# Optimization experiments

Hardware: AMD Instinct MI355X
Metric: run time of the kernel (lower is better)

## Reference

```python
import jax, jax.numpy as jnp
import numpy as np

B, T, C, H = 32, 512, 8, 256  # batch, seq_len, n_channels, HIDDEN_SIZE
G = 4 * H  # gate dim (i, f, g, o)


def setup_inputs() -> dict:
    key = jax.random.key(0)
    ks = jax.random.split(key, 12)
    k_scale = 1.0 / np.sqrt(H)  # PyTorch LSTM/Linear uniform init bound
    u = lambda k, shape: jax.random.uniform(k, shape, jnp.float32, -k_scale, k_scale)
    return {
        "x": jax.random.normal(ks[0], (B, T, C), jnp.float32),
        # per-channel LSTM layer 1 (input_size=1)
        "Wih1": u(ks[1], (C, G, 1)),
        "Whh1": u(ks[2], (C, G, H)),
        "bih1": u(ks[3], (C, G)),
        "bhh1": u(ks[4], (C, G)),
        # per-channel LSTM layer 2 (input_size=H)
        "Wih2": u(ks[5], (C, G, H)),
        "Whh2": u(ks[6], (C, G, H)),
        "bih2": u(ks[7], (C, G)),
        "bhh2": u(ks[8], (C, G)),
        # per-channel Linear(H, 1)
        "Wlin": u(ks[9], (C, H)),
        "blin": u(ks[10], (C,)),
    }


def _lstm_layer(x_proj, Whh):
    """x_proj: [T, C, B, 4H] precomputed input projection + biases.
    Whh: [C, 4H, H]. Returns hidden states [T, C, B, H]."""
    c_dim, b_dim = x_proj.shape[1], x_proj.shape[2]
    h0 = jnp.zeros((c_dim, b_dim, H), x_proj.dtype)
    c0 = jnp.zeros((c_dim, b_dim, H), x_proj.dtype)

    def step(carry, xp_t):
        h, c = carry
        gates = xp_t + jnp.einsum('cbh,cgh->cbg', h, Whh)
        i, f, g, o = jnp.split(gates, 4, axis=-1)  # PyTorch gate order i,f,g,o
        i = jax.nn.sigmoid(i)
        f = jax.nn.sigmoid(f)
        g = jnp.tanh(g)
        o = jax.nn.sigmoid(o)
        c_new = f * c + i * g
        h_new = o * jnp.tanh(c_new)
        return (h_new, c_new), h_new

    _, hs = jax.lax.scan(step, (h0, c0), x_proj)
    return hs  # [T, C, B, H]


def reference(x, Wih1, Whh1, bih1, bhh1, Wih2, Whh2, bih2, bhh2, Wlin, blin):
    # Dropout layers are identity in eval mode.
    # Layer 1: input_size=1 -> input projection is a per-channel scale of x.
    b1 = (bih1 + bhh1)[None, :, None, :]  # [1, C, 1, 4H]
    xp1 = jnp.einsum('btc,cg->tcbg', x, Wih1[:, :, 0]) + b1  # [T, C, B, 4H]
    h1 = _lstm_layer(xp1, Whh1)  # [T, C, B, H]

    # Layer 2
    b2 = (bih2 + bhh2)[None, :, None, :]
    xp2 = jnp.einsum('tcbh,cgh->tcbg', h1, Wih2) + b2
    h2 = _lstm_layer(xp2, Whh2)  # [T, C, B, H]

    # Per-channel Linear(H, 1), concatenated over channel dim.
    out = jnp.einsum('tcbh,ch->btc', h2, Wlin) + blin[None, None, :]
    return out  # [B, T, C]
```

## Files before the change

### kernel.cpp

```cpp
#include <hip/hip_runtime.h>

#define Bn 32
#define Tn 512
#define Cn 8
#define Hn 256
#define Gn 1024
#define NTHR 128
#define SLC  32
#define NBLK (Cn*2*SLC)
#define K2n  (Hn/2)
#define EXU3 (3*Cn*K2n*Bn)
#define GP2  18

typedef __attribute__((ext_vector_type(8))) __bf16 bf16x8;
typedef __attribute__((ext_vector_type(8))) short  short8;
typedef __attribute__((ext_vector_type(4))) float  f32x4;
typedef __attribute__((ext_vector_type(4))) unsigned uintx4;
typedef unsigned long long u64;

__device__ __forceinline__ unsigned bfr(float f) {
    unsigned u = __float_as_uint(f);
    return (u + 0x7fffu + ((u >> 16) & 1u)) >> 16;
}
__device__ __forceinline__ float sigmf(float v)  { return 1.0f / (1.0f + __expf(-v)); }
__device__ __forceinline__ float tanh_f(float v) { return 1.0f - 2.0f / (__expf(2.0f * v) + 1.0f); }

__device__ __forceinline__ f32x4 mf(short8 a, short8 b, f32x4 c) {
    return __builtin_amdgcn_mfma_f32_16x16x32_bf16(
        __builtin_bit_cast(bf16x8, a), __builtin_bit_cast(bf16x8, b), c, 0, 0, 0);
}

__device__ __forceinline__ void splitw(const float* __restrict__ p, short8& hi, short8& lo) {
    short8 h, l;
#pragma unroll
    for (int j = 0; j < 8; ++j) {
        const float v = p[j];
        const unsigned hb = bfr(v);
        h[j] = (short)hb;
        l[j] = (short)bfr(v - __uint_as_float(hb << 16));
    }
    hi = h; lo = l;
}

__device__ __forceinline__ void ast64(u64* p, u64 v) {
    __hip_atomic_store(p, v, __ATOMIC_RELAXED, __HIP_MEMORY_SCOPE_AGENT);
}
__device__ __forceinline__ u64 ald64(const u64* p) {
    return __hip_atomic_load(p, __ATOMIC_RELAXED, __HIP_MEMORY_SCOPE_AGENT);
}

__global__ void __launch_bounds__(NTHR, 1)
lstm_mfma(const float* __restrict__ x,
          const float* __restrict__ Wih1, const float* __restrict__ Whh1,
          const float* __restrict__ bih1, const float* __restrict__ bhh1,
          const float* __restrict__ Wih2, const float* __restrict__ Whh2,
          const float* __restrict__ bih2, const float* __restrict__ bhh2,
          const float* __restrict__ Wlin, const float* __restrict__ blin,
          float* __restrict__ out, void* __restrict__ wsv, int use_part) {
    __shared__ float g1buf[2 * 32 * GP2];
    __shared__ float g2buf[2 * 32 * GP2];

    u64* EX1 = (u64*)wsv;
    u64* EX2 = EX1 + EXU3;
    float* part = (float*)(EX2 + EXU3);

    const int tid  = threadIdx.x;
    const int wg   = blockIdx.x;
    const int c    = wg & 7;
    const int bh   = (wg >> 8) & 1;
    const int s    = (wg >> 3) & 31;
    const int lane = tid & 63;
    const int kg   = tid >> 6;
    const int n    = lane & 15;
    const int quad = lane >> 4;
    const int bn   = bh * 16 + n;

    short8 w1h[2][4], w1l[2][4], w2h[2][4], w2l[2][4], w3h[2][4], w3l[2][4];
#pragma unroll
    for (int mt = 0; mt < 2; ++mt) {
        const int r = mt * 16 + n;
        const size_t g = (size_t)((r >> 3) * Hn + s * 8 + (r & 7));
        const size_t base = (size_t)c * Gn * Hn + g * Hn + kg * 128 + quad * 8;
#pragma unroll
        for (int kk = 0; kk < 4; ++kk) {
            splitw(Whh1 + base + kk * 32, w1h[mt][kk], w1l[mt][kk]);
            splitw(Wih2 + base + kk * 32, w2h[mt][kk], w2l[mt][kk]);
            splitw(Whh2 + base + kk * 32, w3h[mt][kk], w3l[mt][kk]);
        }
    }

    float wi1_r[2][4], bs1_r[2][4], bs2_r[2][4];
#pragma unroll
    for (int mt = 0; mt < 2; ++mt)
#pragma unroll
        for (int reg = 0; reg < 4; ++reg) {
            const int r = mt * 16 + quad * 4 + reg;
            const int g = (r >> 3) * Hn + s * 8 + (r & 7);
            wi1_r[mt][reg] = Wih1[c * Gn + g];
            bs1_r[mt][reg] = bih1[c * Gn + g] + bhh1[c * Gn + g];
            bs2_r[mt][reg] = bih2[c * Gn + g] + bhh2[c * Gn + g];
        }

    const int jj = tid & 7;
    const int bb = tid >> 3;
    const int gb = bh * 16 + bb;
    const float wl = Wlin[c * Hn + s * 8 + jj];
    const float bl = blin[c];

    float c1 = 0.0f, c2 = 0.0f;

    int wb = 0;
    int rb = 2;
    unsigned ctag = 1;
    unsigned ptag = 3;

    for (int t = 0; t <= Tn; ++t) {
        const bool doA = (t < Tn);
        const bool doB = (t >= 1);

        const float xv = doA ? x[(bn * Tn + t) * Cn + c] : 0.0f;

        const u64* E1 = EX1 + (size_t)(rb * Cn + c) * K2n * Bn;
        const u64* E2 = EX2 + (size_t)(rb * Cn + c) * K2n * Bn;
        const unsigned em = (ptag & 1u) | ((ptag & 2u) << 15);
        const bool chk1 = (t >= 1);
        const bool chk2 = (t >= 2);
        short8 f2h[4], f2l[4], f1h[4], f1l[4];
        bool got1 = false, got2 = false;
        for (;;) {
            unsigned bad1 = 0, bad2 = 0;
            if (!got2) {
#pragma unroll
                for (int kk = 0; kk < 4; ++kk) {
                    uintx4 a2h, a2l;
#pragma unroll
                    for (int j2 = 0; j2 < 4; ++j2) {
                        const int k2 = kg * 64 + kk * 16 + quad * 4 + j2;
                        const u64 v2 = ald64(E2 + k2 * Bn + bn);
                        a2h[j2] = (unsigned)v2;
                        a2l[j2] = (unsigned)(v2 >> 32);
                        bad2 |= (a2l[j2] ^ em) & 0x00010001u;
                    }
                    f2h[kk] = __builtin_bit_cast(short8, a2h);
                    f2l[kk] = __builtin_bit_cast(short8, a2l);
                }
            }
            if (!got1) {
#pragma unroll
                for (int kk = 0; kk < 4; ++kk) {
                    uintx4 a1h, a1l;
#pragma unroll
                    for (int j2 = 0; j2 < 4; ++j2) {
                        const int k2 = kg * 64 + kk * 16 + quad * 4 + j2;
                        const u64 v1 = ald64(E1 + k2 * Bn + bn);
                        a1h[j2] = (unsigned)v1;
                        a1l[j2] = (unsigned)(v1 >> 32);
                        bad1 |= (a1l[j2] ^ em) & 0x00010001u;
                    }
                    f1h[kk] = __builtin_bit_cast(short8, a1h);
                    f1l[kk] = __builtin_bit_cast(short8, a1l);
                }
            }
            if (!got2) got2 = !chk2 || __all((int)(bad2 == 0));
            if (!got1) got1 = !chk1 || __all((int)(bad1 == 0));
            if (got1 && got2) break;
            __builtin_amdgcn_s_sleep(1);
        }

        f32x4 a1a[2] = {{0,0,0,0},{0,0,0,0}}, a1x[2] = {{0,0,0,0},{0,0,0,0}};
        f32x4 a2a[2] = {{0,0,0,0},{0,0,0,0}}, a2x[2] = {{0,0,0,0},{0,0,0,0}};
#pragma unroll
        for (int kk = 0; kk < 4; ++kk)
#pragma unroll
            for (int mt = 0; mt < 2; ++mt) {
                a2a[mt] = mf(w3h[mt][kk], f2h[kk], a2a[mt]);
                a2x[mt] = mf(w3l[mt][kk], f2h[kk], mf(w3h[mt][kk], f2l[kk], a2x[mt]));
                a1a[mt] = mf(w1h[mt][kk], f1h[kk], a1a[mt]);
                a1x[mt] = mf(w1l[mt][kk], f1h[kk], mf(w1h[mt][kk], f1l[kk], a1x[mt]));
                a2a[mt] = mf(w2h[mt][kk], f1h[kk], a2a[mt]);
                a2x[mt] = mf(w2l[mt][kk], f1h[kk], mf(w2h[mt][kk], f1l[kk], a2x[mt]));
            }

#pragma unroll
        for (int mt = 0; mt < 2; ++mt)
#pragma unroll
            for (int reg = 0; reg < 4; ++reg) {
                const int r = mt * 16 + quad * 4 + reg;
                const int off = (kg * 32 + r) * GP2 + n;
                float e1 = a1a[mt][reg] + a1x[mt][reg];
                float e2 = a2a[mt][reg] + a2x[mt][reg];
                if (kg == 0) {
                    e1 += xv * wi1_r[mt][reg] + bs1_r[mt][reg];
                    e2 += bs2_r[mt][reg];
                }
                g1buf[off] = e1;
                g2buf[off] = e2;
            }
        __syncthreads();

        const unsigned cm = (ctag & 1u) | ((ctag & 2u) << 15);

        if (doA) {
            const float iv = sigmf (g1buf[jj * GP2 + bb]        + g1buf[(32 + jj) * GP2 + bb]);
            const float fv = sigmf (g1buf[(8 + jj) * GP2 + bb]  + g1buf[(40 + jj) * GP2 + bb]);
            const float gv = tanh_f(g1buf[(16 + jj) * GP2 + bb] + g1buf[(48 + jj) * GP2 + bb]);
            const float ov = sigmf (g1buf[(24 + jj) * GP2 + bb] + g1buf[(56 + jj) * GP2 + bb]);
            c1 = fv * c1 + iv * gv;
            const float h1v = ov * tanh_f(c1);
            const unsigned hb = bfr(h1v);
            const unsigned lb = bfr(h1v - __uint_as_float(hb << 16));
            const unsigned packed = (hb << 16) | lb;
            const unsigned nbp = (unsigned)__shfl_xor((int)packed, 1, 64);
            if ((jj & 1) == 0) {
                const unsigned hip = (packed >> 16) | (nbp & 0xffff0000u);
                unsigned lop = (packed & 0xffffu) | (nbp << 16);
                lop = (lop & 0xFFFEFFFEu) | cm;
                const int k2 = s * 4 + (jj >> 1);
                ast64(EX1 + (size_t)(wb * Cn + c) * K2n * Bn + k2 * Bn + gb,
                      (u64)hip | ((u64)lop << 32));
            }
        }
        if (doB) {
            const float iv = sigmf (g2buf[jj * GP2 + bb]        + g2buf[(32 + jj) * GP2 + bb]);
            const float fv = sigmf (g2buf[(8 + jj) * GP2 + bb]  + g2buf[(40 + jj) * GP2 + bb]);
            const float gv = tanh_f(g2buf[(16 + jj) * GP2 + bb] + g2buf[(48 + jj) * GP2 + bb]);
            const float ov = sigmf (g2buf[(24 + jj) * GP2 + bb] + g2buf[(56 + jj) * GP2 + bb]);
            c2 = fv * c2 + iv * gv;
            const float h2v = ov * tanh_f(c2);
            const unsigned hb = bfr(h2v);
            const unsigned lb = bfr(h2v - __uint_as_float(hb << 16));
            const unsigned packed = (hb << 16) | lb;
            const unsigned nbp = (unsigned)__shfl_xor((int)packed, 1, 64);
            if ((jj & 1) == 0) {
                const unsigned hip = (packed >> 16) | (nbp & 0xffff0000u);
                unsigned lop = (packed & 0xffffu) | (nbp << 16);
                lop = (lop & 0xFFFEFFFEu) | cm;
                const int k2 = s * 4 + (jj >> 1);
                ast64(EX2 + (size_t)(wb * Cn + c) * K2n * Bn + k2 * Bn + gb,
                      (u64)hip | ((u64)lop << 32));
            }

            float pv = h2v * wl;
            pv += __shfl_xor(pv, 1, 64);
            pv += __shfl_xor(pv, 2, 64);
            pv += __shfl_xor(pv, 4, 64);
            if (jj == 0) {
                if (use_part) {
                    part[(((t - 1) * Cn + c) * SLC + s) * Bn + gb] = pv;
                } else {
                    atomicAdd(&out[(gb * Tn + (t - 1)) * Cn + c], pv + (s == 0 ? bl : 0.0f));
                }
            }
        }

        __syncthreads();

        rb = wb; wb = (wb == 2) ? 0 : wb + 1;
        ptag = ctag; ctag = (ctag == 3u) ? 1u : ctag + 1u;
    }
}

__global__ void reduce_out(const float* __restrict__ part, const float* __restrict__ blin,
                           float* __restrict__ out) {
    const int t = blockIdx.x;
    const int c = threadIdx.x >> 5;
    const int b = threadIdx.x & 31;
    float v = blin[c];
#pragma unroll
    for (int s = 0; s < SLC; ++s) v += part[((t * Cn + c) * SLC + s) * Bn + b];
    out[(b * Tn + t) * Cn + c] = v;
}

extern "C" void kernel_launch(void* const* d_in, const int* in_sizes, int n_in,
                              void* d_out, int out_size, void* d_ws, size_t ws_size,
                              hipStream_t stream) {
    const float* x    = (const float*)d_in[0];
    const float* Wih1 = (const float*)d_in[1];
    const float* Whh1 = (const float*)d_in[2];
    const float* bih1 = (const float*)d_in[3];
    const float* bhh1 = (const float*)d_in[4];
    const float* Wih2 = (const float*)d_in[5];
    const float* Whh2 = (const float*)d_in[6];
    const float* bih2 = (const float*)d_in[7];
    const float* bhh2 = (const float*)d_in[8];
    const float* Wlin = (const float*)d_in[9];
    const float* blin = (const float*)d_in[10];
    float* out = (float*)d_out;

    const size_t h_bytes    = (size_t)2 * EXU3 * sizeof(u64);
    const size_t part_bytes = (size_t)Tn * Cn * SLC * Bn * sizeof(float);
    const int use_part = (ws_size >= h_bytes + part_bytes) ? 1 : 0;

    hipMemsetAsync(d_ws, 0, h_bytes, stream);
    if (!use_part)
        hipMemsetAsync(d_out, 0, (size_t)out_size * sizeof(float), stream);

    lstm_mfma<<<NBLK, NTHR, 0, stream>>>(
        x, Wih1, Whh1, bih1, bhh1, Wih2, Whh2, bih2, bhh2, Wlin, blin, out, d_ws, use_part);

    if (use_part) {
        const float* part = (const float*)((const char*)d_ws + h_bytes);
        reduce_out<<<Tn, Cn * Bn, 0, stream>>>(part, blin, out);
    }
}
```

Before: 2.011 ms.

## Halve workgroup count with 256-thread blocks covering 16 hidden units each

Each workgroup now uses four waves and owns 16 hidden units per gate instead of 8, so the grid shrinks from 512 to 256 blocks and each block produces a wider slice of h per step. The exchange buffer goes from three to four slots, with buffer and tag indices computed from t rather than rotated. The layer-2 exchange store is skipped on the last step. The aim is fewer participants in the per-step cross-block spin-wait and less exchange traffic per unit of work, at the cost of more work per block on each serial step.

```diff
diff --git a/kernel.cpp b/kernel.cpp
--- a/kernel.cpp
+++ b/kernel.cpp
@@ -5,11 +5,12 @@
 #define Cn 8
 #define Hn 256
 #define Gn 1024
-#define NTHR 128
-#define SLC  32
+#define NTHR 256
+#define SLC  16
 #define NBLK (Cn*2*SLC)
 #define K2n  (Hn/2)
-#define EXU3 (3*Cn*K2n*Bn)
+#define BUFS 4
+#define EXU  (BUFS*Cn*K2n*Bn)
 #define GP2  18
 
 typedef __attribute__((ext_vector_type(8))) __bf16 bf16x8;
@@ -57,20 +58,22 @@
           const float* __restrict__ bih2, const float* __restrict__ bhh2,
           const float* __restrict__ Wlin, const float* __restrict__ blin,
           float* __restrict__ out, void* __restrict__ wsv, int use_part) {
-    __shared__ float g1buf[2 * 32 * GP2];
-    __shared__ float g2buf[2 * 32 * GP2];
+    __shared__ float g1buf[2 * 64 * GP2];
+    __shared__ float g2buf[2 * 64 * GP2];
 
     u64* EX1 = (u64*)wsv;
-    u64* EX2 = EX1 + EXU3;
-    float* part = (float*)(EX2 + EXU3);
+    u64* EX2 = EX1 + EXU;
+    float* part = (float*)(EX2 + EXU);
 
     const int tid  = threadIdx.x;
     const int wg   = blockIdx.x;
     const int c    = wg & 7;
-    const int bh   = (wg >> 8) & 1;
-    const int s    = (wg >> 3) & 31;
+    const int s    = (wg >> 3) & 15;
+    const int bh   = (wg >> 7) & 1;
     const int lane = tid & 63;
-    const int kg   = tid >> 6;
+    const int wid  = tid >> 6;
+    const int kg   = wid & 1;
+    const int mh   = wid >> 1;
     const int n    = lane & 15;
     const int quad = lane >> 4;
     const int bn   = bh * 16 + n;
@@ -78,8 +81,8 @@
     short8 w1h[2][4], w1l[2][4], w2h[2][4], w2l[2][4], w3h[2][4], w3l[2][4];
 #pragma unroll
     for (int mt = 0; mt < 2; ++mt) {
-        const int r = mt * 16 + n;
-        const size_t g = (size_t)((r >> 3) * Hn + s * 8 + (r & 7));
+        const int r = mh * 32 + mt * 16 + n;
+        const size_t g = (size_t)((r >> 4) * Hn + s * 16 + (r & 15));
         const size_t base = (size_t)c * Gn * Hn + g * Hn + kg * 128 + quad * 8;
 #pragma unroll
         for (int kk = 0; kk < 4; ++kk) {
@@ -94,29 +97,28 @@
     for (int mt = 0; mt < 2; ++mt)
 #pragma unroll
         for (int reg = 0; reg < 4; ++reg) {
-            const int r = mt * 16 + quad * 4 + reg;
-            const int g = (r >> 3) * Hn + s * 8 + (r & 7);
+            const int r = mh * 32 + mt * 16 + quad * 4 + reg;
+            const int g = (r >> 4) * Hn + s * 16 + (r & 15);
             wi1_r[mt][reg] = Wih1[c * Gn + g];
             bs1_r[mt][reg] = bih1[c * Gn + g] + bhh1[c * Gn + g];
             bs2_r[mt][reg] = bih2[c * Gn + g] + bhh2[c * Gn + g];
         }
 
-    const int jj = tid & 7;
-    const int bb = tid >> 3;
+    const int jj = tid & 15;
+    const int bb = tid >> 4;
     const int gb = bh * 16 + bb;
-    const float wl = Wlin[c * Hn + s * 8 + jj];
+    const float wl = Wlin[c * Hn + s * 16 + jj];
     const float bl = blin[c];
 
     float c1 = 0.0f, c2 = 0.0f;
-
-    int wb = 0;
-    int rb = 2;
-    unsigned ctag = 1;
-    unsigned ptag = 3;
 
     for (int t = 0; t <= Tn; ++t) {
         const bool doA = (t < Tn);
         const bool doB = (t >= 1);
+        const int wb = t & 3;
+        const int rb = (t + 3) & 3;
+        const unsigned ctag = (unsigned)(t % 3) + 1u;
+        const unsigned ptag = (unsigned)((t + 2) % 3) + 1u;
 
         const float xv = doA ? x[(bn * Tn + t) * Cn + c] : 0.0f;
 
@@ -185,8 +187,8 @@
         for (int mt = 0; mt < 2; ++mt)
 #pragma unroll
             for (int reg = 0; reg < 4; ++reg) {
-                const int r = mt * 16 + quad * 4 + reg;
-                const int off = (kg * 32 + r) * GP2 + n;
+                const int r = mh * 32 + mt * 16 + quad * 4 + reg;
+                const int off = (kg * 64 + r) * GP2 + n;
                 float e1 = a1a[mt][reg] + a1x[mt][reg];
                 float e2 = a2a[mt][reg] + a2x[mt][reg];
                 if (kg == 0) {
@@ -201,10 +203,10 @@
         const unsigned cm = (ctag & 1u) | ((ctag & 2u) << 15);
 
         if (doA) {
-            const float iv = sigmf (g1buf[jj * GP2 + bb]        + g1buf[(32 + jj) * GP2 + bb]);
-            const float fv = sigmf (g1buf[(8 + jj) * GP2 + bb]  + g1buf[(40 + jj) * GP2 + bb]);
-            const float gv = tanh_f(g1buf[(16 + jj) * GP2 + bb] + g1buf[(48 + jj) * GP2 + bb]);
-            const float ov = sigmf (g1buf[(24 + jj) * GP2 + bb] + g1buf[(56 + jj) * GP2 + bb]);
+            const float iv = sigmf (g1buf[jj * GP2 + bb]        + g1buf[(64 + jj) * GP2 + bb]);
+            const float fv = sigmf (g1buf[(16 + jj) * GP2 + bb] + g1buf[(80 + jj) * GP2 + bb]);
+            const float gv = tanh_f(g1buf[(32 + jj) * GP2 + bb] + g1buf[(96 + jj) * GP2 + bb]);
+            const float ov = sigmf (g1buf[(48 + jj) * GP2 + bb] + g1buf[(112 + jj) * GP2 + bb]);
             c1 = fv * c1 + iv * gv;
             const float h1v = ov * tanh_f(c1);
             const unsigned hb = bfr(h1v);
@@ -215,35 +217,40 @@
                 const unsigned hip = (packed >> 16) | (nbp & 0xffff0000u);
                 unsigned lop = (packed & 0xffffu) | (nbp << 16);
                 lop = (lop & 0xFFFEFFFEu) | cm;
-                const int k2 = s * 4 + (jj >> 1);
+                const int k2 = s * 8 + (jj >> 1);
                 ast64(EX1 + (size_t)(wb * Cn + c) * K2n * Bn + k2 * Bn + gb,
                       (u64)hip | ((u64)lop << 32));
             }
         }
         if (doB) {
-            const float iv = sigmf (g2buf[jj * GP2 + bb]        + g2buf[(32 + jj) * GP2 + bb]);
-            const float fv = sigmf (g2buf[(8 + jj) * GP2 + bb]  + g2buf[(40 + jj) * GP2 + bb]);
-            const float gv = tanh_f(g2buf[(16 + jj) * GP2 + bb] + g2buf[(48 + jj) * GP2 + bb]);
-            const float ov = sigmf (g2buf[(24 + jj) * GP2 + bb] + g2buf[(56 + jj) * GP2 + bb]);
+            const float iv = sigmf (g2buf[jj * GP2 + bb]        + g2buf[(64 + jj) * GP2 + bb]);
+            const float fv = sigmf (g2buf[(16 + jj) * GP2 + bb] + g2buf[(80 + jj) * GP2 + bb]);
+            const float gv = tanh_f(g2buf[(32 + jj) * GP2 + bb] + g2buf[(96 + jj) * GP2 + bb]);
+            const float ov = sigmf (g2buf[(48 + jj) * GP2 + bb] + g2buf[(112 + jj) * GP2 + bb]);
             c2 = fv * c2 + iv * gv;
             const float h2v = ov * tanh_f(c2);
-            const unsigned hb = bfr(h2v);
-            const unsigned lb = bfr(h2v - __uint_as_float(hb << 16));
-            const unsigned packed = (hb << 16) | lb;
-            const unsigned nbp = (unsigned)__shfl_xor((int)packed, 1, 64);
-            if ((jj & 1) == 0) {
-                const unsigned hip = (packed >> 16) | (nbp & 0xffff0000u);
-                unsigned lop = (packed & 0xffffu) | (nbp << 16);
-                lop = (lop & 0xFFFEFFFEu) | cm;
-                const int k2 = s * 4 + (jj >> 1);
-                ast64(EX2 + (size_t)(wb * Cn + c) * K2n * Bn + k2 * Bn + gb,
-                      (u64)hip | ((u64)lop << 32));
+            if (t < Tn) {
+                const unsigned hb = bfr(h2v);
+                const unsigned lb = bfr(h2v - __uint_as_float(hb << 16));
+                const unsigned packed = (hb << 16) | lb;
+                const unsigned nbp = (unsigned)__shfl_xor((int)packed, 1, 64);
+                if ((jj & 1) == 0) {
+                    const unsigned hip = (packed >> 16) | (nbp & 0xffff0000u);
+                    unsigned lop = (packed & 0xffffu) | (nbp << 16);
+                    lop = (lop & 0xFFFEFFFEu) | cm;
+                    const int k2 = s * 8 + (jj >> 1);
+                    ast64(EX2 + (size_t)(wb * Cn + c) * K2n * Bn + k2 * Bn + gb,
+                          (u64)hip | ((u64)lop << 32));
+                }
+            } else {
+                (void)__shfl_xor(0, 1, 64);
             }
 
             float pv = h2v * wl;
             pv += __shfl_xor(pv, 1, 64);
             pv += __shfl_xor(pv, 2, 64);
             pv += __shfl_xor(pv, 4, 64);
+            pv += __shfl_xor(pv, 8, 64);
             if (jj == 0) {
                 if (use_part) {
                     part[(((t - 1) * Cn + c) * SLC + s) * Bn + gb] = pv;
@@ -254,9 +261,6 @@
         }
 
         __syncthreads();
-
-        rb = wb; wb = (wb == 2) ? 0 : wb + 1;
-        ptag = ctag; ctag = (ctag == 3u) ? 1u : ctag + 1u;
     }
 }
 
@@ -287,7 +291,7 @@
     const float* blin = (const float*)d_in[10];
     float* out = (float*)d_out;
 
-    const size_t h_bytes    = (size_t)2 * EXU3 * sizeof(u64);
+    const size_t h_bytes    = (size_t)2 * EXU * sizeof(u64);
     const size_t part_bytes = (size_t)Tn * Cn * SLC * Bn * sizeof(float);
     const int use_part = (ws_size >= h_bytes + part_bytes) ? 1 : 0;
 
```

New measurement: 1.865 ms. 7.2% less time.
